# Kernel tuning notes

Measured on AMD Instinct MI355X. Metric: run time of the kernel, lower is better.

## Reference

```python
import jax, jax.numpy as jnp
import numpy as np

T_STEPS = 100
T_EMB = 16
EPS = 1e-8


def sin_emb(t, dim):
    # sinusoidal_time_embedding: [cos(t*f), sin(t*f)] with f = exp(-log(1e4)*i/half)
    half = dim // 2
    freqs = jnp.exp(-jnp.log(jnp.float32(10000.0)) * jnp.arange(half, dtype=jnp.float32) / half)
    a = t.astype(jnp.float32)[:, None] * freqs[None, :]
    return jnp.concatenate([jnp.cos(a), jnp.sin(a)], axis=-1)


def lstm_layer(x_tbf, W_ih, W_hh, b):
    # x_tbf: [T, B, F]; torch gate order i, f, g, o
    B = x_tbf.shape[1]
    H = W_hh.shape[1]

    def step(carry, x_t):
        h, c = carry
        g = x_t @ W_ih.T + h @ W_hh.T + b
        i, f, gg, o = jnp.split(g, 4, axis=-1)
        c = jax.nn.sigmoid(f) * c + jax.nn.sigmoid(i) * jnp.tanh(gg)
        h = jax.nn.sigmoid(o) * jnp.tanh(c)
        return (h, c), h

    z = jnp.zeros((B, H), x_tbf.dtype)
    (h, c), ys = jax.lax.scan(step, (z, z), x_tbf)
    return ys, h


def _forward(x_hist, x_future, y0, turb_idx, pred_steps, init_noise, turb_emb,
             W_ih0, W_hh0, b_ih0, b_hh0, W_ih1, W_hh1, b_ih1, b_hh1,
             W1, b1, W2, b2, W3, b3):
    betas = jnp.linspace(1e-4, 0.02, T_STEPS).astype(jnp.float32)
    alphas = 1.0 - betas
    alpha_bars = jnp.cumprod(alphas)

    B = x_hist.shape[0]
    emb = turb_emb[turb_idx]  # [B, E]
    eh = jnp.broadcast_to(emb[:, None, :], (B, x_hist.shape[1], emb.shape[1]))
    ef = jnp.broadcast_to(emb[:, None, :], (B, x_future.shape[1], emb.shape[1]))
    xh = jnp.concatenate([x_hist, eh], axis=-1).transpose(1, 0, 2)    # [T_in, B, F+E]
    xf = jnp.concatenate([x_future, ef], axis=-1).transpose(1, 0, 2)  # [P, B, exo+E]

    ys0, _ = lstm_layer(xh, W_ih0, W_hh0, b_ih0 + b_hh0)
    _, enc_out = lstm_layer(ys0, W_ih1, W_hh1, b_ih1 + b_hh1)         # [B, H] = h[-1]

    def mlp(x):
        h = jax.nn.relu(x @ W1.T + b1)
        h = jax.nn.relu(h @ W2.T + b2)
        return h @ W3.T + b3

    def ar_step(prev_y, xs):
        exo_t, step, y_init = xs
        cond = jnp.concatenate([enc_out, exo_t, prev_y], axis=1)  # [B, cond_dim]
        h_e = sin_emb(jnp.full((B,), step), T_EMB)

        def dstep(y, t):
            t_e = sin_emb(jnp.full((B,), t), T_EMB)
            eps_hat = mlp(jnp.concatenate([cond, y, t_e, h_e], axis=1))  # [B,1]
            b_t, a_t, ab_t = betas[t], alphas[t], alpha_bars[t]
            pred_x0 = (y - jnp.sqrt(1.0 - ab_t) * eps_hat) / (jnp.sqrt(ab_t) + EPS)
            mean = (y - b_t / (jnp.sqrt(1.0 - ab_t) + EPS) * eps_hat) / (jnp.sqrt(a_t) + EPS)
            # eval mode -> deterministic sampling: posterior noise term is zero
            return jnp.where(t == 0, pred_x0, mean), None

        y, _ = jax.lax.scan(dstep, y_init, jnp.arange(T_STEPS - 1, -1, -1))
        return y, y[:, 0]

    _, seq = jax.lax.scan(ar_step, y0, (xf, jnp.arange(pred_steps), init_noise))
    return seq.T[:, :, None]  # [B, pred_steps, 1]


def setup_inputs() -> dict:
    key = jax.random.key(0)
    ks = list(jax.random.split(key, 24))
    kit = iter(ks)
    B, T_IN, F_IN, EXO, EMB, PRED, HID, NTURB = 1024, 96, 8, 6, 16, 8, 128, 100
    in0 = F_IN + EMB                 # 24
    cond_dim = HID + EXO + EMB + 1   # 151
    in_mlp = cond_dim + 1 + T_EMB + T_EMB  # 184

    def nrm(shape, s=0.05):
        return jax.random.normal(next(kit), shape, jnp.float32) * s

    return {
        'x_hist': jax.random.normal(next(kit), (B, T_IN, F_IN), jnp.float32),
        'x_future': jax.random.normal(next(kit), (B, PRED, EXO), jnp.float32),
        'y0': jnp.zeros((B, 1), jnp.float32),
        'turb_idx': jax.random.randint(next(kit), (B,), 0, NTURB),
        'pred_steps': PRED,
        'init_noise': jax.random.normal(next(kit), (PRED, B, 1), jnp.float32),
        'turb_emb': nrm((NTURB, EMB), 0.1),
        'W_ih0': nrm((4 * HID, in0)), 'W_hh0': nrm((4 * HID, HID)),
        'b_ih0': jnp.zeros((4 * HID,), jnp.float32), 'b_hh0': jnp.zeros((4 * HID,), jnp.float32),
        'W_ih1': nrm((4 * HID, HID)), 'W_hh1': nrm((4 * HID, HID)),
        'b_ih1': jnp.zeros((4 * HID,), jnp.float32), 'b_hh1': jnp.zeros((4 * HID,), jnp.float32),
        'W1': nrm((HID, in_mlp)), 'b1': jnp.zeros((HID,), jnp.float32),
        'W2': nrm((HID, HID)), 'b2': jnp.zeros((HID,), jnp.float32),
        'W3': nrm((1, HID)), 'b3': jnp.zeros((1,), jnp.float32),
    }


def reference(x_hist, x_future, y0, turb_idx, pred_steps, init_noise, turb_emb,
              W_ih0, W_hh0, b_ih0, b_hh0, W_ih1, W_hh1, b_ih1, b_hh1,
              W1, b1, W2, b2, W3, b3):
    return _forward(x_hist, x_future, y0, turb_idx, pred_steps, init_noise, turb_emb,
                    W_ih0, W_hh0, b_ih0, b_hh0, W_ih1, W_hh1, b_ih1, b_hh1,
                    W1, b1, W2, b2, W3, b3)
```

## Files before the change

kernel.cpp:

```cpp
#include <hip/hip_runtime.h>
#include <hip/hip_fp16.h>
#include <stdint.h>


typedef __attribute__((ext_vector_type(2))) _Float16 half2_t;
typedef __attribute__((ext_vector_type(8))) _Float16 v8h;
typedef __attribute__((ext_vector_type(4))) float v4f;

#define DEV __device__ __forceinline__

DEV uint32_t pack2f(float a, float b) {
  __half ha = __float2half_rn(a), hb = __float2half_rn(b);
  return (uint32_t)__half_as_ushort(ha) | ((uint32_t)__half_as_ushort(hb) << 16);
}

DEV float2 up2(uint32_t u) {
  half2_t h = __builtin_bit_cast(half2_t, u);
  return make_float2((float)h.x, (float)h.y);
}

DEV float fast_ex2(float x) {
#if __has_builtin(__builtin_amdgcn_exp2f)
  return __builtin_amdgcn_exp2f(x);
#else
  return exp2f(x);
#endif
}
DEV float fast_rcp(float x) {
#if __has_builtin(__builtin_amdgcn_rcpf)
  return __builtin_amdgcn_rcpf(x);
#else
  return 1.f / x;
#endif
}
DEV float sigm(float x) { return fast_rcp(1.f + fast_ex2(-1.4426950408889634f * x)); }
DEV float tanh_f(float x) {
  return 2.f * fast_rcp(1.f + fast_ex2(-2.8853900817779268f * x)) - 1.f;
}

DEV uint32_t pk_add(uint32_t a, uint32_t b) {
  return __builtin_bit_cast(uint32_t,
      __builtin_bit_cast(half2_t, a) + __builtin_bit_cast(half2_t, b));
}

DEV uint32_t pk_relufma(uint32_t w, uint32_t y, uint32_t b) {
  half2_t r = __builtin_bit_cast(half2_t, w) * __builtin_bit_cast(half2_t, y) +
              __builtin_bit_cast(half2_t, b);
  half2_t z = {(_Float16)0.f, (_Float16)0.f};
#if __has_builtin(__builtin_elementwise_max)
  r = __builtin_elementwise_max(r, z);
#else
  uint32_t u = __builtin_bit_cast(uint32_t, r);
  uint32_t mask = ((u >> 15) & 1u) * 0xFFFFu | ((u >> 31) & 1u) * 0xFFFF0000u;
  r = __builtin_bit_cast(half2_t, u & ~mask);
#endif
  return __builtin_bit_cast(uint32_t, r);
}

DEV uint32_t pk_max0(uint32_t a) {
  half2_t z = {(_Float16)0.f, (_Float16)0.f};
#if __has_builtin(__builtin_elementwise_max)
  return __builtin_bit_cast(uint32_t,
      __builtin_elementwise_max(__builtin_bit_cast(half2_t, a), z));
#else
  uint32_t mask = ((a >> 15) & 1u) * 0xFFFFu | ((a >> 31) & 1u) * 0xFFFF0000u;
  return a & ~mask;
#endif
}

DEV uint32_t cvtpk(float y) {
#if __has_builtin(__builtin_amdgcn_cvt_pkrtz)
  return __builtin_bit_cast(uint32_t, __builtin_amdgcn_cvt_pkrtz(y, y));
#else
  return pack2f(y, y);
#endif
}

DEV uint32_t cvtpk2(float a, float b) {
#if __has_builtin(__builtin_amdgcn_cvt_pkrtz)
  return __builtin_bit_cast(uint32_t, __builtin_amdgcn_cvt_pkrtz(a, b));
#else
  return pack2f(a, b);
#endif
}

DEV half2_t pk_fma2(uint32_t a, uint32_t b, half2_t c) {
  return __builtin_bit_cast(half2_t, a) * __builtin_bit_cast(half2_t, b) + c;
}

static constexpr size_t OFF_XH  = 0;
static constexpr size_t OFF_W0  = 4718592;
static constexpr size_t OFF_BS0 = 4882432;
static constexpr size_t OFF_W1L = 4884480;
static constexpr size_t OFF_BS1 = 5146624;
static constexpr size_t OFF_W2P = 5148672;
static constexpr size_t OFF_ENC = 5181440;
static constexpr size_t OFF_YS0 = 5705728;

__global__ void k_prep_xh(const float* __restrict__ xh, const int* __restrict__ tix,
                          const float* __restrict__ temb, uint32_t* __restrict__ out) {
  int idx = blockIdx.x * 256 + threadIdx.x;
  if (idx >= 96 * 1024 * 12) return;
  int m = idx % 12;
  int tb = idx / 12;
  int b = tb & 1023, t = tb >> 10;
  int k0 = 2 * m, k1 = k0 + 1;
  float v0 = (k0 < 8) ? xh[(b * 96 + t) * 8 + k0] : temb[tix[b] * 16 + (k0 - 8)];
  float v1 = (k1 < 8) ? xh[(b * 96 + t) * 8 + k1] : temb[tix[b] * 16 + (k1 - 8)];
  out[idx] = pack2f(v0, v1);
}

__global__ void k_prep_w(const float* __restrict__ Wih0, const float* __restrict__ Whh0,
                         const float* __restrict__ bih0, const float* __restrict__ bhh0,
                         const float* __restrict__ Wih1, const float* __restrict__ Whh1,
                         const float* __restrict__ bih1, const float* __restrict__ bhh1,
                         const float* __restrict__ W2,
                         uint32_t* __restrict__ w0p, uint32_t* __restrict__ w1p,
                         uint32_t* __restrict__ w2p, float* __restrict__ bs0,
                         float* __restrict__ bs1) {
  int idx = blockIdx.x * 256 + threadIdx.x;
  if (idx < 40960) {
    int w = idx / 5120;
    int r = idx % 5120;
    int T = r / 1280; r %= 1280;
    int f = r / 256;  r %= 256;
    int l = r >> 2, c = r & 3;
    int m = l & 15, qf = l >> 4;
    int g = (m & 3) * 128 + w * 16 + (m >> 2) * 4 + T;
    int k0 = f * 32 + qf * 8 + 2 * c, k1 = k0 + 1;
    float a = (k0 < 24) ? Wih0[g * 24 + k0] : ((k0 < 152) ? Whh0[g * 128 + k0 - 24] : 0.f);
    float b = (k1 < 24) ? Wih0[g * 24 + k1] : ((k1 < 152) ? Whh0[g * 128 + k1 - 24] : 0.f);
    w0p[idx] = pack2f(a, b);
  } else if (idx < 106496) {
    int i = idx - 40960;
    int w = i / 8192;
    int r = i % 8192;
    int T = r / 2048; r %= 2048;
    int f = r / 256;  r %= 256;
    int l = r >> 2, c = r & 3;
    int m = l & 15, qf = l >> 4;
    int g = (m & 3) * 128 + w * 16 + (m >> 2) * 4 + T;
    int k0 = f * 32 + qf * 8 + 2 * c, k1 = k0 + 1;
    float a = (k0 < 128) ? Wih1[g * 128 + k0] : Whh1[g * 128 + k0 - 128];
    float b = (k1 < 128) ? Wih1[g * 128 + k1] : Whh1[g * 128 + k1 - 128];
    w1p[i] = pack2f(a, b);
  } else if (idx < 114688) {
    int i = idx - 106496;
    w2p[i] = pack2f(W2[2 * i], W2[2 * i + 1]);
  } else if (idx < 115200) {
    int i = idx - 114688;
    bs0[i] = bih0[i] + bhh0[i];
  } else if (idx < 115712) {
    int i = idx - 115200;
    bs1[i] = bih1[i] + bhh1[i];
  }
}

__global__ __launch_bounds__(512, 2) void k_lstm0(const uint32_t* __restrict__ xh16,
                                                  const uint32_t* __restrict__ w0A,
                                                  const float* __restrict__ bs0,
                                                  __half* __restrict__ ys0) {
  __shared__ __align__(16) __half inb[2][16][160];
  const int tid = threadIdx.x;
  const int w = tid >> 6, l = tid & 63;
  const int n = l & 15, ql = l >> 4;
  const int ju = w * 16 + ql * 4;
  const int bbase = blockIdx.x * 16;

  uint4 Af[4][5];
#pragma unroll
  for (int T = 0; T < 4; T++)
#pragma unroll
    for (int f = 0; f < 5; f++)
      Af[T][f] = ((const uint4*)w0A)[((w * 4 + T) * 5 + f) * 64 + l];
  float bias[4][4];
#pragma unroll
  for (int T = 0; T < 4; T++)
#pragma unroll
    for (int r = 0; r < 4; r++) bias[T][r] = bs0[r * 128 + ju + T];

  for (int i = tid; i < 2560; i += 512) ((uint32_t*)inb)[i] = 0u;
  __syncthreads();
  if (tid < 192) {
    int b = tid / 12, m = tid % 12;
    ((uint32_t*)&inb[0][b][0])[m] = xh16[(0 * 1024 + bbase + b) * 12 + m];
  }
  float cst[4] = {0.f, 0.f, 0.f, 0.f};
  __syncthreads();

  for (int t = 0; t < 96; t++) {
    const int cur = t & 1, nxt = cur ^ 1;
    uint32_t sx = 0;
    int sb = 0, sm = 0;
    if (t < 95 && tid < 192) {
      sb = tid / 12; sm = tid % 12;
      sx = xh16[((t + 1) * 1024 + bbase + sb) * 12 + sm];
    }
    v4f acc[4];
#pragma unroll
    for (int T = 0; T < 4; T++) acc[T] = (v4f){0.f, 0.f, 0.f, 0.f};
#pragma unroll
    for (int f = 0; f < 5; f++) {
      uint4 bu = *(const uint4*)&inb[cur][n][f * 32 + ql * 8];
      v8h Bv = __builtin_bit_cast(v8h, bu);
#pragma unroll
      for (int T = 0; T < 4; T++)
        acc[T] = __builtin_amdgcn_mfma_f32_16x16x32_f16(
            __builtin_bit_cast(v8h, Af[T][f]), Bv, acc[T], 0, 0, 0);
    }
    float hv[4];
#pragma unroll
    for (int T = 0; T < 4; T++) {
      float gi = acc[T][0] + bias[T][0];
      float gf = acc[T][1] + bias[T][1];
      float gg = acc[T][2] + bias[T][2];
      float go = acc[T][3] + bias[T][3];
      float c = sigm(gf) * cst[T] + sigm(gi) * tanh_f(gg);
      cst[T] = c;
      hv[T] = sigm(go) * tanh_f(c);
    }
    uint32_t h01 = pack2f(hv[0], hv[1]), h23 = pack2f(hv[2], hv[3]);
    *(uint2*)&inb[nxt][n][24 + ju] = make_uint2(h01, h23);
    *(uint2*)((__half*)ys0 + (size_t)(t * 1024 + bbase + n) * 128 + ju) = make_uint2(h01, h23);
    if (t < 95 && tid < 192) ((uint32_t*)&inb[nxt][sb][0])[sm] = sx;
    __syncthreads();
  }
}

__global__ __launch_bounds__(512, 2) void k_lstm1(const uint32_t* __restrict__ ys0u,
                                                  const uint32_t* __restrict__ w1A,
                                                  const float* __restrict__ bs1,
                                                  float* __restrict__ enc) {
  __shared__ __align__(16) __half inb[2][16][264];
  const int tid = threadIdx.x;
  const int w = tid >> 6, l = tid & 63;
  const int n = l & 15, ql = l >> 4;
  const int ju = w * 16 + ql * 4;
  const int bbase = blockIdx.x * 16;
  const int sb = tid >> 5, sc = tid & 31;

  uint4 Af[4][8];
#pragma unroll
  for (int T = 0; T < 4; T++)
#pragma unroll
    for (int f = 0; f < 8; f++)
      Af[T][f] = ((const uint4*)w1A)[((w * 4 + T) * 8 + f) * 64 + l];
  float bias[4][4];
#pragma unroll
  for (int T = 0; T < 4; T++)
#pragma unroll
    for (int r = 0; r < 4; r++) bias[T][r] = bs1[r * 128 + ju + T];

  for (int i = tid; i < 4224; i += 512) ((uint32_t*)inb)[i] = 0u;
  __syncthreads();
  {
    uint2 v = ((const uint2*)ys0u)[(size_t)(0 * 1024 + bbase + sb) * 32 + sc];
    *(uint2*)&inb[0][sb][sc * 4] = v;
  }
  float cst[4] = {0.f, 0.f, 0.f, 0.f};
  __syncthreads();

  for (int t = 0; t < 96; t++) {
    const int cur = t & 1, nxt = cur ^ 1;
    uint2 sv = make_uint2(0u, 0u);
    if (t < 95)
      sv = ((const uint2*)ys0u)[(size_t)((t + 1) * 1024 + bbase + sb) * 32 + sc];
    v4f acc[4];
#pragma unroll
    for (int T = 0; T < 4; T++) acc[T] = (v4f){0.f, 0.f, 0.f, 0.f};
#pragma unroll
    for (int f = 0; f < 8; f++) {
      uint4 bu = *(const uint4*)&inb[cur][n][f * 32 + ql * 8];
      v8h Bv = __builtin_bit_cast(v8h, bu);
#pragma unroll
      for (int T = 0; T < 4; T++)
        acc[T] = __builtin_amdgcn_mfma_f32_16x16x32_f16(
            __builtin_bit_cast(v8h, Af[T][f]), Bv, acc[T], 0, 0, 0);
    }
    float hv[4];
#pragma unroll
    for (int T = 0; T < 4; T++) {
      float gi = acc[T][0] + bias[T][0];
      float gf = acc[T][1] + bias[T][1];
      float gg = acc[T][2] + bias[T][2];
      float go = acc[T][3] + bias[T][3];
      float c = sigm(gf) * cst[T] + sigm(gi) * tanh_f(gg);
      cst[T] = c;
      hv[T] = sigm(go) * tanh_f(c);
    }
    *(uint2*)&inb[nxt][n][128 + ju] = make_uint2(pack2f(hv[0], hv[1]), pack2f(hv[2], hv[3]));
    if (t < 95) *(uint2*)&inb[nxt][sb][sc * 4] = sv;
    if (t == 95)
      *(float4*)&enc[(size_t)(bbase + n) * 128 + ju] = make_float4(hv[0], hv[1], hv[2], hv[3]);
    __syncthreads();
  }
}

__global__ __launch_bounds__(256, 1) void k_diff(
    const float* __restrict__ xfut, const float* __restrict__ y0,
    const int* __restrict__ tix, const float* __restrict__ noise,
    const float* __restrict__ temb, const float* __restrict__ W1,
    const float* __restrict__ b1, const float* __restrict__ b2,
    const float* __restrict__ W3, const float* __restrict__ b3,
    const uint32_t* __restrict__ w2p, const float* __restrict__ enc,
    float* __restrict__ out) {
  __shared__ uint32_t W1sL[128 * 65];
  __shared__ uint32_t W1xL[128 * 29];
  __shared__ uint32_t encPL[16 * 65];
  __shared__ uint32_t embPL[16 * 9];
  __shared__ float teL[100][16];
  __shared__ float2 ccL[100];
  __shared__ __align__(16) __half tprojL[100 * 128];
  __shared__ __half hprojL[8 * 128];
  __shared__ uint32_t encdL[256 * 17];
  __shared__ __align__(16) float partL[2][16][20];

  const int tid = threadIdx.x;
  const int w = tid >> 6, l = tid & 63;
  const int m = l & 15, q = l >> 4;
  const int gbase = blockIdx.x * 16;

  for (int i = tid; i < 128 * 64; i += 256) {
    int r = i >> 6, c = i & 63;
    W1sL[r * 65 + c] = pack2f(W1[r * 184 + 2 * c], W1[r * 184 + 2 * c + 1]);
  }
  for (int i = tid; i < 128 * 28; i += 256) {
    int r = i / 28, c = i % 28;
    W1xL[r * 29 + c] = pack2f(W1[r * 184 + 128 + 2 * c], W1[r * 184 + 129 + 2 * c]);
  }
  for (int i = tid; i < 16 * 64; i += 256) {
    int bq = i >> 6, c = i & 63;
    encPL[bq * 65 + c] = pack2f(enc[(gbase + bq) * 128 + 2 * c],
                                enc[(gbase + bq) * 128 + 2 * c + 1]);
  }
  for (int i = tid; i < 16 * 8; i += 256) {
    int bq = i >> 3, c = i & 7;
    const float* er = temb + tix[gbase + bq] * 16;
    embPL[bq * 9 + c] = pack2f(er[2 * c], er[2 * c + 1]);
  }
  for (int p = tid; p < 1600; p += 256) {
    int tt = p >> 4, i = p & 15;
    float f = expf(-logf(10000.f) * (float)(i & 7) / 8.f);
    float a = (float)tt * f;
    teL[tt][i] = (i < 8) ? cosf(a) : sinf(a);
  }
  for (int qq = tid; qq < 100; qq += 256) {
    float ab = 1.f, beta = 0.f;
    for (int i = 0; i <= qq; i++) {
      beta = 1e-4f + (0.02f - 1e-4f) * (float)i / 99.f;
      ab *= (1.f - beta);
    }
    float cs, cd;
    if (qq == 0) { cs = sqrtf(1.f - ab); cd = 1.f / (sqrtf(ab) + 1e-8f); }
    else { cs = beta / (sqrtf(1.f - ab) + 1e-8f); cd = 1.f / (sqrtf(1.f - beta) + 1e-8f); }
    ccL[qq] = make_float2(cs, cd);
  }
  __syncthreads();

  {
    int k = tid & 127, hs = tid >> 7;
    float wte[16], whe[16];
#pragma unroll
    for (int i = 0; i < 8; i++) {
      float2 a = up2(W1xL[k * 29 + 12 + i]);
      wte[2 * i] = a.x; wte[2 * i + 1] = a.y;
      float2 bqq = up2(W1xL[k * 29 + 20 + i]);
      whe[2 * i] = bqq.x; whe[2 * i + 1] = bqq.y;
    }
    for (int tt = hs * 50; tt < hs * 50 + 50; tt++) {
      float s = 0.f;
#pragma unroll
      for (int i = 0; i < 16; i++) s += wte[i] * teL[tt][i];
      tprojL[tt * 128 + k] = __float2half_rn(s);
    }
    if (hs == 0) {
      for (int ss = 0; ss < 8; ss++) {
        float s = 0.f;
#pragma unroll
        for (int i = 0; i < 16; i++) s += whe[i] * teL[ss][i];
        hprojL[ss * 128 + k] = __float2half_rn(s);
      }
    }
  }

  for (int pi = 0; pi < 16; pi++) {
    int k0 = (pi >> 2) * 32 + q * 8 + (pi & 3) * 2;
    half2_t a0 = {(_Float16)0.f, (_Float16)0.f};
    half2_t a1 = a0;
    const uint32_t* wr0 = &W1sL[k0 * 65];
    const uint32_t* wr1 = &W1sL[(k0 + 1) * 65];
    const uint32_t* ep = &encPL[m * 65];
#pragma unroll 8
    for (int c = 0; c < 64; c++) {
      half2_t e = __builtin_bit_cast(half2_t, ep[c]);
      a0 += __builtin_bit_cast(half2_t, wr0[c]) * e;
      a1 += __builtin_bit_cast(half2_t, wr1[c]) * e;
    }
#pragma unroll
    for (int c = 0; c < 8; c++) {
      half2_t e = __builtin_bit_cast(half2_t, embPL[m * 9 + c]);
      a0 += __builtin_bit_cast(half2_t, W1xL[k0 * 29 + 3 + c]) * e;
      a1 += __builtin_bit_cast(half2_t, W1xL[(k0 + 1) * 29 + 3 + c]) * e;
    }
    float e0 = b1[k0] + (float)a0.x + (float)a0.y;
    float e1 = b1[k0 + 1] + (float)a1.x + (float)a1.y;
    encdL[tid * 17 + pi] = pack2f(e0, e1);
  }

  uint4 Bf[2][4];
  {
    const uint4* w2u4 = (const uint4*)w2p;
#pragma unroll
    for (int j = 0; j < 2; j++)
#pragma unroll
      for (int f = 0; f < 4; f++)
        Bf[j][f] = w2u4[((2 * w + j) * 16 + m) * 16 + f * 4 + q];
  }
  uint32_t b2P[4], w3P[4];
#pragma unroll
  for (int j = 0; j < 2; j++) {
    int tt = 2 * w + j;
    b2P[2 * j]     = pack2f(b2[tt * 16 + q * 4 + 0], b2[tt * 16 + q * 4 + 1]);
    b2P[2 * j + 1] = pack2f(b2[tt * 16 + q * 4 + 2], b2[tt * 16 + q * 4 + 3]);
    w3P[2 * j]     = pack2f(W3[tt * 16 + q * 4 + 0], W3[tt * 16 + q * 4 + 1]);
    w3P[2 * j + 1] = pack2f(W3[tt * 16 + q * 4 + 2], W3[tt * 16 + q * 4 + 3]);
  }
  const float b3v = b3[0];
  const int pslot = w * 4 + q;

  uint32_t w1yP[16];
#pragma unroll
  for (int pi = 0; pi < 16; pi++) {
    int k0 = (pi >> 2) * 32 + q * 8 + (pi & 3) * 2;
    uint32_t ua = W1xL[k0 * 29 + 11];
    uint32_t ub = W1xL[(k0 + 1) * 29 + 11];
    w1yP[pi] = (ua >> 16) | (ub & 0xFFFF0000u);
  }

  float prev_y = y0[gbase + m];
  __syncthreads();

  float y = 0.f;
  float2 ccv = make_float2(0.f, 0.f);
  uint32_t bph[16], bt[16];
  const v4f zf = (v4f){0.f, 0.f, 0.f, 0.f};

#define DSTEP(t_, PB)                                                          \
  do {                                                                         \
    const int tn_ = ((t_) > 0) ? (t_) - 1 : 0;                                 \
    const uint4* tb_ = (const uint4*)(tprojL + tn_ * 128 + q * 8);             \
    uint4 t0 = tb_[0], t1 = tb_[4], t2 = tb_[8], t3 = tb_[12];                 \
    float2 ccn_ = ccL[tn_];                                                    \
    const uint32_t yP = cvtpk(y);                                              \
    uint4 au[4];                                                               \
    _Pragma("unroll")                                                          \
    for (int f = 0; f < 4; f++) {                                              \
      au[f].x = pk_relufma(w1yP[4 * f + 0], yP, bt[4 * f + 0]);                \
      au[f].y = pk_relufma(w1yP[4 * f + 1], yP, bt[4 * f + 1]);                \
      au[f].z = pk_relufma(w1yP[4 * f + 2], yP, bt[4 * f + 2]);                \
      au[f].w = pk_relufma(w1yP[4 * f + 3], yP, bt[4 * f + 3]);                \
    }                                                                          \
                             \
    v4f a0 = __builtin_amdgcn_mfma_f32_16x16x32_f16(                           \
        __builtin_bit_cast(v8h, Bf[0][0]), __builtin_bit_cast(v8h, au[0]), zf, 0, 0, 0); \
    v4f b0 = __builtin_amdgcn_mfma_f32_16x16x32_f16(                           \
        __builtin_bit_cast(v8h, Bf[0][1]), __builtin_bit_cast(v8h, au[1]), zf, 0, 0, 0); \
    v4f a1 = __builtin_amdgcn_mfma_f32_16x16x32_f16(                           \
        __builtin_bit_cast(v8h, Bf[1][0]), __builtin_bit_cast(v8h, au[0]), zf, 0, 0, 0); \
    v4f b1x = __builtin_amdgcn_mfma_f32_16x16x32_f16(                          \
        __builtin_bit_cast(v8h, Bf[1][1]), __builtin_bit_cast(v8h, au[1]), zf, 0, 0, 0); \
    a0 = __builtin_amdgcn_mfma_f32_16x16x32_f16(                               \
        __builtin_bit_cast(v8h, Bf[0][2]), __builtin_bit_cast(v8h, au[2]), a0, 0, 0, 0); \
    b0 = __builtin_amdgcn_mfma_f32_16x16x32_f16(                               \
        __builtin_bit_cast(v8h, Bf[0][3]), __builtin_bit_cast(v8h, au[3]), b0, 0, 0, 0); \
    a1 = __builtin_amdgcn_mfma_f32_16x16x32_f16(                               \
        __builtin_bit_cast(v8h, Bf[1][2]), __builtin_bit_cast(v8h, au[2]), a1, 0, 0, 0); \
    b1x = __builtin_amdgcn_mfma_f32_16x16x32_f16(                              \
        __builtin_bit_cast(v8h, Bf[1][3]), __builtin_bit_cast(v8h, au[3]), b1x, 0, 0, 0); \
    v4f c0 = a0 + b0, c1 = a1 + b1x;                                           \
              \
    half2_t run = {(_Float16)0.f, (_Float16)0.f};                              \
    {                                                                          \
      uint32_t h01 = pk_max0(pk_add(cvtpk2(c0[0], c0[1]), b2P[0]));            \
      uint32_t h23 = pk_max0(pk_add(cvtpk2(c0[2], c0[3]), b2P[1]));            \
      run = pk_fma2(h01, w3P[0], run);                                         \
      run = pk_fma2(h23, w3P[1], run);                                         \
      uint32_t g01 = pk_max0(pk_add(cvtpk2(c1[0], c1[1]), b2P[2]));            \
      uint32_t g23 = pk_max0(pk_add(cvtpk2(c1[2], c1[3]), b2P[3]));            \
      run = pk_fma2(g01, w3P[2], run);                                         \
      run = pk_fma2(g23, w3P[3], run);                                         \
    }                                                                          \
    partL[PB][m][pslot] = (float)run.x + (float)run.y;                         \
                                         \
    bt[0] = pk_add(bph[0], t0.x);   bt[1] = pk_add(bph[1], t0.y);              \
    bt[2] = pk_add(bph[2], t0.z);   bt[3] = pk_add(bph[3], t0.w);              \
    bt[4] = pk_add(bph[4], t1.x);   bt[5] = pk_add(bph[5], t1.y);              \
    bt[6] = pk_add(bph[6], t1.z);   bt[7] = pk_add(bph[7], t1.w);              \
    bt[8] = pk_add(bph[8], t2.x);   bt[9] = pk_add(bph[9], t2.y);              \
    bt[10] = pk_add(bph[10], t2.z); bt[11] = pk_add(bph[11], t2.w);            \
    bt[12] = pk_add(bph[12], t3.x); bt[13] = pk_add(bph[13], t3.y);            \
    bt[14] = pk_add(bph[14], t3.z); bt[15] = pk_add(bph[15], t3.w);            \
    __syncthreads();                                                           \
    const v4f* pl_ = (const v4f*)&partL[PB][m][0];                             \
    v4f p0_ = pl_[0], p1_ = pl_[1], p2_ = pl_[2], p3_ = pl_[3];                \
    v4f ps_ = (p0_ + p1_) + (p2_ + p3_);                                       \
    float eps_ = b3v + ((ps_[0] + ps_[1]) + (ps_[2] + ps_[3]));                \
    y = (y - ccv.x * eps_) * ccv.y;                                            \
    ccv = ccn_;                                                                \
  } while (0)

  for (int s = 0; s < 8; s++) {
    float yn = noise[s * 1024 + gbase + m];
    float xf[6];
#pragma unroll
    for (int i = 0; i < 6; i++) xf[i] = xfut[((gbase + m) * 8 + s) * 6 + i];
#pragma unroll
    for (int pi = 0; pi < 16; pi++) {
      int k0 = (pi >> 2) * 32 + q * 8 + (pi & 3) * 2;
      float2 ed = up2(encdL[tid * 17 + pi]);
      float e0 = ed.x, e1 = ed.y;
#pragma unroll
      for (int c = 0; c < 3; c++) {
        float2 w0v = up2(W1xL[k0 * 29 + c]);
        float2 w1v = up2(W1xL[(k0 + 1) * 29 + c]);
        e0 += w0v.x * xf[2 * c] + w0v.y * xf[2 * c + 1];
        e1 += w1v.x * xf[2 * c] + w1v.y * xf[2 * c + 1];
      }
      e0 += up2(W1xL[k0 * 29 + 11]).x * prev_y;
      e1 += up2(W1xL[(k0 + 1) * 29 + 11]).x * prev_y;
      e0 += (float)hprojL[s * 128 + k0];
      e1 += (float)hprojL[s * 128 + k0 + 1];
      bph[pi] = pack2f(e0, e1);
    }

    y = yn;
    {
      const uint4* tb = (const uint4*)(tprojL + 99 * 128 + q * 8);
      uint4 t0 = tb[0], t1 = tb[4], t2 = tb[8], t3 = tb[12];
      bt[0] = pk_add(bph[0], t0.x);   bt[1] = pk_add(bph[1], t0.y);
      bt[2] = pk_add(bph[2], t0.z);   bt[3] = pk_add(bph[3], t0.w);
      bt[4] = pk_add(bph[4], t1.x);   bt[5] = pk_add(bph[5], t1.y);
      bt[6] = pk_add(bph[6], t1.z);   bt[7] = pk_add(bph[7], t1.w);
      bt[8] = pk_add(bph[8], t2.x);   bt[9] = pk_add(bph[9], t2.y);
      bt[10] = pk_add(bph[10], t2.z); bt[11] = pk_add(bph[11], t2.w);
      bt[12] = pk_add(bph[12], t3.x); bt[13] = pk_add(bph[13], t3.y);
      bt[14] = pk_add(bph[14], t3.z); bt[15] = pk_add(bph[15], t3.w);
    }
    ccv = ccL[99];

    for (int it = 0; it < 50; it++) {
      DSTEP(99 - 2 * it, 0);
      DSTEP(98 - 2 * it, 1);
    }

    if (w == 0 && l < 16) out[(gbase + l) * 8 + s] = y;
    prev_y = y;
  }
#undef DSTEP
}

extern "C" void kernel_launch(void* const* d_in, const int* in_sizes, int n_in,
                              void* d_out, int out_size, void* d_ws, size_t ws_size,
                              hipStream_t stream) {
  const float* x_hist    = (const float*)d_in[0];
  const float* x_future  = (const float*)d_in[1];
  const float* y0        = (const float*)d_in[2];
  const int*   turb_idx  = (const int*)d_in[3];
  const float* init_noise = (const float*)d_in[5];
  const float* turb_emb  = (const float*)d_in[6];
  const float* W_ih0     = (const float*)d_in[7];
  const float* W_hh0     = (const float*)d_in[8];
  const float* b_ih0     = (const float*)d_in[9];
  const float* b_hh0     = (const float*)d_in[10];
  const float* W_ih1     = (const float*)d_in[11];
  const float* W_hh1     = (const float*)d_in[12];
  const float* b_ih1     = (const float*)d_in[13];
  const float* b_hh1     = (const float*)d_in[14];
  const float* W1        = (const float*)d_in[15];
  const float* b1        = (const float*)d_in[16];
  const float* W2        = (const float*)d_in[17];
  const float* b2        = (const float*)d_in[18];
  const float* W3        = (const float*)d_in[19];
  const float* b3        = (const float*)d_in[20];

  char* ws = (char*)d_ws;
  uint32_t* xh16 = (uint32_t*)(ws + OFF_XH);
  uint32_t* w0p  = (uint32_t*)(ws + OFF_W0);
  float*    bs0  = (float*)(ws + OFF_BS0);
  uint32_t* w1p  = (uint32_t*)(ws + OFF_W1L);
  float*    bs1  = (float*)(ws + OFF_BS1);
  uint32_t* w2p  = (uint32_t*)(ws + OFF_W2P);
  float*    encf = (float*)(ws + OFF_ENC);
  __half*   ys0h = (__half*)(ws + OFF_YS0);

  k_prep_xh<<<4608, 256, 0, stream>>>(x_hist, turb_idx, turb_emb, xh16);
  k_prep_w<<<452, 256, 0, stream>>>(W_ih0, W_hh0, b_ih0, b_hh0,
                                    W_ih1, W_hh1, b_ih1, b_hh1,
                                    W2, w0p, w1p, w2p, bs0, bs1);
  k_lstm0<<<64, 512, 0, stream>>>(xh16, w0p, bs0, ys0h);
  k_lstm1<<<64, 512, 0, stream>>>((const uint32_t*)ys0h, w1p, bs1, encf);
  k_diff<<<64, 256, 0, stream>>>(x_future, y0, turb_idx, init_noise, turb_emb,
                                 W1, b1, b2, W3, b3, w2p, encf, (float*)d_out);
}
```

Baseline: 638.5 us.

## Precompute diffusion time projections in prep kernel and halve diffusion block size

The time-embedding projections, step-embedding projections and schedule coefficients move out of the per-block setup of k_diff into the prep kernel, which writes them to workspace. k_diff now reads them from global memory (cached) inside the denoising loop. The diffusion kernel drops from 4 to 2 waves per block, and each wave now does 4 MFMA tiles of W2 instead of 2. This shrinks the cross-wave reduction and the barrier cost on every serial denoising step. The risks are extra global-load latency on the critical serial path and more register pressure per wave.

```diff
diff --git a/kernel.cpp b/kernel.cpp
--- a/kernel.cpp
+++ b/kernel.cpp
@@ -96,6 +96,9 @@
 static constexpr size_t OFF_W2P = 5148672;
 static constexpr size_t OFF_ENC = 5181440;
 static constexpr size_t OFF_YS0 = 5705728;
+static constexpr size_t OFF_TPJ = 30871552;
+static constexpr size_t OFF_HPJ = 30897152;
+static constexpr size_t OFF_CC  = 30899200;
 
 __global__ void k_prep_xh(const float* __restrict__ xh, const int* __restrict__ tix,
                           const float* __restrict__ temb, uint32_t* __restrict__ out) {
@@ -114,10 +117,11 @@
                          const float* __restrict__ bih0, const float* __restrict__ bhh0,
                          const float* __restrict__ Wih1, const float* __restrict__ Whh1,
                          const float* __restrict__ bih1, const float* __restrict__ bhh1,
-                         const float* __restrict__ W2,
+                         const float* __restrict__ W2, const float* __restrict__ W1,
                          uint32_t* __restrict__ w0p, uint32_t* __restrict__ w1p,
                          uint32_t* __restrict__ w2p, float* __restrict__ bs0,
-                         float* __restrict__ bs1) {
+                         float* __restrict__ bs1, uint32_t* __restrict__ tpj,
+                         uint32_t* __restrict__ hpj, float2* __restrict__ ccg) {
   int idx = blockIdx.x * 256 + threadIdx.x;
   if (idx < 40960) {
     int w = idx / 5120;
@@ -153,6 +157,59 @@
   } else if (idx < 115712) {
     int i = idx - 115200;
     bs1[i] = bih1[i] + bhh1[i];
+  } else if (idx < 122112) {
+    int i = idx - 115712;
+    int t = i / 64;
+    int r = i % 64;
+    int q = r / 16, pi = r % 16;
+    int k0 = (pi >> 2) * 32 + q * 8 + (pi & 3) * 2;
+    float te[16];
+#pragma unroll
+    for (int j = 0; j < 8; j++) {
+      float f = expf(-logf(10000.f) * (float)j / 8.f);
+      float a = (float)t * f;
+      te[j] = cosf(a);
+      te[j + 8] = sinf(a);
+    }
+    float s0 = 0.f, s1 = 0.f;
+#pragma unroll
+    for (int j = 0; j < 16; j++) {
+      s0 += W1[k0 * 184 + 152 + j] * te[j];
+      s1 += W1[(k0 + 1) * 184 + 152 + j] * te[j];
+    }
+    tpj[i] = pack2f((float)__half2float(__float2half_rn(s0)),
+                    (float)__half2float(__float2half_rn(s1)));
+  } else if (idx < 122624) {
+    int i = idx - 122112;
+    int s = i / 64;
+    int kp = i % 64;
+    float te[16];
+#pragma unroll
+    for (int j = 0; j < 8; j++) {
+      float f = expf(-logf(10000.f) * (float)j / 8.f);
+      float a = (float)s * f;
+      te[j] = cosf(a);
+      te[j + 8] = sinf(a);
+    }
+    float s0 = 0.f, s1 = 0.f;
+#pragma unroll
+    for (int j = 0; j < 16; j++) {
+      s0 += W1[(2 * kp) * 184 + 168 + j] * te[j];
+      s1 += W1[(2 * kp + 1) * 184 + 168 + j] * te[j];
+    }
+    hpj[i] = pack2f((float)__half2float(__float2half_rn(s0)),
+                    (float)__half2float(__float2half_rn(s1)));
+  } else if (idx < 122724) {
+    int qq = idx - 122624;
+    float ab = 1.f, beta = 0.f;
+    for (int i = 0; i <= qq; i++) {
+      beta = 1e-4f + (0.02f - 1e-4f) * (float)i / 99.f;
+      ab *= (1.f - beta);
+    }
+    float cs, cd;
+    if (qq == 0) { cs = sqrtf(1.f - ab); cd = 1.f / (sqrtf(ab) + 1e-8f); }
+    else { cs = beta / (sqrtf(1.f - ab) + 1e-8f); cd = 1.f / (sqrtf(1.f - beta) + 1e-8f); }
+    ccg[qq] = make_float2(cs, cd);
   }
 }
 
@@ -296,92 +353,47 @@
   }
 }
 
-__global__ __launch_bounds__(256, 1) void k_diff(
+__global__ __launch_bounds__(128, 1) void k_diff(
     const float* __restrict__ xfut, const float* __restrict__ y0,
     const int* __restrict__ tix, const float* __restrict__ noise,
     const float* __restrict__ temb, const float* __restrict__ W1,
     const float* __restrict__ b1, const float* __restrict__ b2,
     const float* __restrict__ W3, const float* __restrict__ b3,
     const uint32_t* __restrict__ w2p, const float* __restrict__ enc,
-    float* __restrict__ out) {
+    const uint32_t* __restrict__ tpj, const uint32_t* __restrict__ hpj,
+    const float2* __restrict__ ccG, float* __restrict__ out) {
   __shared__ uint32_t W1sL[128 * 65];
   __shared__ uint32_t W1xL[128 * 29];
   __shared__ uint32_t encPL[16 * 65];
   __shared__ uint32_t embPL[16 * 9];
-  __shared__ float teL[100][16];
-  __shared__ float2 ccL[100];
-  __shared__ __align__(16) __half tprojL[100 * 128];
-  __shared__ __half hprojL[8 * 128];
-  __shared__ uint32_t encdL[256 * 17];
-  __shared__ __align__(16) float partL[2][16][20];
+  __shared__ uint32_t encdL[128 * 17];
+  __shared__ __align__(16) float partL[2][16][12];
 
   const int tid = threadIdx.x;
   const int w = tid >> 6, l = tid & 63;
   const int m = l & 15, q = l >> 4;
   const int gbase = blockIdx.x * 16;
-
-  for (int i = tid; i < 128 * 64; i += 256) {
+  const uint4* tpj4 = (const uint4*)tpj;
+
+  for (int i = tid; i < 128 * 64; i += 128) {
     int r = i >> 6, c = i & 63;
     W1sL[r * 65 + c] = pack2f(W1[r * 184 + 2 * c], W1[r * 184 + 2 * c + 1]);
   }
-  for (int i = tid; i < 128 * 28; i += 256) {
+  for (int i = tid; i < 128 * 28; i += 128) {
     int r = i / 28, c = i % 28;
     W1xL[r * 29 + c] = pack2f(W1[r * 184 + 128 + 2 * c], W1[r * 184 + 129 + 2 * c]);
   }
-  for (int i = tid; i < 16 * 64; i += 256) {
+  for (int i = tid; i < 16 * 64; i += 128) {
     int bq = i >> 6, c = i & 63;
     encPL[bq * 65 + c] = pack2f(enc[(gbase + bq) * 128 + 2 * c],
                                 enc[(gbase + bq) * 128 + 2 * c + 1]);
   }
-  for (int i = tid; i < 16 * 8; i += 256) {
+  for (int i = tid; i < 16 * 8; i += 128) {
     int bq = i >> 3, c = i & 7;
     const float* er = temb + tix[gbase + bq] * 16;
     embPL[bq * 9 + c] = pack2f(er[2 * c], er[2 * c + 1]);
   }
-  for (int p = tid; p < 1600; p += 256) {
-    int tt = p >> 4, i = p & 15;
-    float f = expf(-logf(10000.f) * (float)(i & 7) / 8.f);
-    float a = (float)tt * f;
-    teL[tt][i] = (i < 8) ? cosf(a) : sinf(a);
-  }
-  for (int qq = tid; qq < 100; qq += 256) {
-    float ab = 1.f, beta = 0.f;
-    for (int i = 0; i <= qq; i++) {
-      beta = 1e-4f + (0.02f - 1e-4f) * (float)i / 99.f;
-      ab *= (1.f - beta);
-    }
-    float cs, cd;
-    if (qq == 0) { cs = sqrtf(1.f - ab); cd = 1.f / (sqrtf(ab) + 1e-8f); }
-    else { cs = beta / (sqrtf(1.f - ab) + 1e-8f); cd = 1.f / (sqrtf(1.f - beta) + 1e-8f); }
-    ccL[qq] = make_float2(cs, cd);
-  }
   __syncthreads();
-
-  {
-    int k = tid & 127, hs = tid >> 7;
-    float wte[16], whe[16];
-#pragma unroll
-    for (int i = 0; i < 8; i++) {
-      float2 a = up2(W1xL[k * 29 + 12 + i]);
-      wte[2 * i] = a.x; wte[2 * i + 1] = a.y;
-      float2 bqq = up2(W1xL[k * 29 + 20 + i]);
-      whe[2 * i] = bqq.x; whe[2 * i + 1] = bqq.y;
-    }
-    for (int tt = hs * 50; tt < hs * 50 + 50; tt++) {
-      float s = 0.f;
-#pragma unroll
-      for (int i = 0; i < 16; i++) s += wte[i] * teL[tt][i];
-      tprojL[tt * 128 + k] = __float2half_rn(s);
-    }
-    if (hs == 0) {
-      for (int ss = 0; ss < 8; ss++) {
-        float s = 0.f;
-#pragma unroll
-        for (int i = 0; i < 16; i++) s += whe[i] * teL[ss][i];
-        hprojL[ss * 128 + k] = __float2half_rn(s);
-      }
-    }
-  }
 
   for (int pi = 0; pi < 16; pi++) {
     int k0 = (pi >> 2) * 32 + q * 8 + (pi & 3) * 2;
@@ -407,19 +419,19 @@
     encdL[tid * 17 + pi] = pack2f(e0, e1);
   }
 
-  uint4 Bf[2][4];
+  uint4 Bf[4][4];
   {
     const uint4* w2u4 = (const uint4*)w2p;
 #pragma unroll
-    for (int j = 0; j < 2; j++)
+    for (int j = 0; j < 4; j++)
 #pragma unroll
       for (int f = 0; f < 4; f++)
-        Bf[j][f] = w2u4[((2 * w + j) * 16 + m) * 16 + f * 4 + q];
-  }
-  uint32_t b2P[4], w3P[4];
-#pragma unroll
-  for (int j = 0; j < 2; j++) {
-    int tt = 2 * w + j;
+        Bf[j][f] = w2u4[((4 * w + j) * 16 + m) * 16 + f * 4 + q];
+  }
+  uint32_t b2P[8], w3P[8];
+#pragma unroll
+  for (int j = 0; j < 4; j++) {
+    int tt = 4 * w + j;
     b2P[2 * j]     = pack2f(b2[tt * 16 + q * 4 + 0], b2[tt * 16 + q * 4 + 1]);
     b2P[2 * j + 1] = pack2f(b2[tt * 16 + q * 4 + 2], b2[tt * 16 + q * 4 + 3]);
     w3P[2 * j]     = pack2f(W3[tt * 16 + q * 4 + 0], W3[tt * 16 + q * 4 + 1]);
@@ -448,9 +460,9 @@
 #define DSTEP(t_, PB)                                                          \
   do {                                                                         \
     const int tn_ = ((t_) > 0) ? (t_) - 1 : 0;                                 \
-    const uint4* tb_ = (const uint4*)(tprojL + tn_ * 128 + q * 8);             \
-    uint4 t0 = tb_[0], t1 = tb_[4], t2 = tb_[8], t3 = tb_[12];                 \
-    float2 ccn_ = ccL[tn_];                                                    \
+    const uint4* tg_ = tpj4 + (size_t)(tn_ * 4 + q) * 4;    \
+    uint4 t0 = tg_[0], t1 = tg_[1], t2 = tg_[2], t3 = tg_[3];                  \
+    float2 ccn_ = ccG[tn_];                                                    \
     const uint32_t yP = cvtpk(y);                                              \
     uint4 au[4];                                                               \
     _Pragma("unroll")                                                          \
@@ -460,37 +472,49 @@
       au[f].z = pk_relufma(w1yP[4 * f + 2], yP, bt[4 * f + 2]);                \
       au[f].w = pk_relufma(w1yP[4 * f + 3], yP, bt[4 * f + 3]);                \
     }                                                                          \
-                             \
-    v4f a0 = __builtin_amdgcn_mfma_f32_16x16x32_f16(                           \
-        __builtin_bit_cast(v8h, Bf[0][0]), __builtin_bit_cast(v8h, au[0]), zf, 0, 0, 0); \
-    v4f b0 = __builtin_amdgcn_mfma_f32_16x16x32_f16(                           \
-        __builtin_bit_cast(v8h, Bf[0][1]), __builtin_bit_cast(v8h, au[1]), zf, 0, 0, 0); \
-    v4f a1 = __builtin_amdgcn_mfma_f32_16x16x32_f16(                           \
-        __builtin_bit_cast(v8h, Bf[1][0]), __builtin_bit_cast(v8h, au[0]), zf, 0, 0, 0); \
-    v4f b1x = __builtin_amdgcn_mfma_f32_16x16x32_f16(                          \
-        __builtin_bit_cast(v8h, Bf[1][1]), __builtin_bit_cast(v8h, au[1]), zf, 0, 0, 0); \
-    a0 = __builtin_amdgcn_mfma_f32_16x16x32_f16(                               \
-        __builtin_bit_cast(v8h, Bf[0][2]), __builtin_bit_cast(v8h, au[2]), a0, 0, 0, 0); \
-    b0 = __builtin_amdgcn_mfma_f32_16x16x32_f16(                               \
-        __builtin_bit_cast(v8h, Bf[0][3]), __builtin_bit_cast(v8h, au[3]), b0, 0, 0, 0); \
-    a1 = __builtin_amdgcn_mfma_f32_16x16x32_f16(                               \
-        __builtin_bit_cast(v8h, Bf[1][2]), __builtin_bit_cast(v8h, au[2]), a1, 0, 0, 0); \
-    b1x = __builtin_amdgcn_mfma_f32_16x16x32_f16(                              \
-        __builtin_bit_cast(v8h, Bf[1][3]), __builtin_bit_cast(v8h, au[3]), b1x, 0, 0, 0); \
-    v4f c0 = a0 + b0, c1 = a1 + b1x;                                           \
+                            \
+    v4f aA[4], aB[4];                                                          \
+    _Pragma("unroll")                                                          \
+    for (int j = 0; j < 4; j++)                                                \
+      aA[j] = __builtin_amdgcn_mfma_f32_16x16x32_f16(                          \
+          __builtin_bit_cast(v8h, Bf[j][0]), __builtin_bit_cast(v8h, au[0]),   \
+          zf, 0, 0, 0);                                                        \
+    _Pragma("unroll")                                                          \
+    for (int j = 0; j < 4; j++)                                                \
+      aB[j] = __builtin_amdgcn_mfma_f32_16x16x32_f16(                          \
+          __builtin_bit_cast(v8h, Bf[j][1]), __builtin_bit_cast(v8h, au[1]),   \
+          zf, 0, 0, 0);                                                        \
+    _Pragma("unroll")                                                          \
+    for (int j = 0; j < 4; j++)                                                \
+      aA[j] = __builtin_amdgcn_mfma_f32_16x16x32_f16(                          \
+          __builtin_bit_cast(v8h, Bf[j][2]), __builtin_bit_cast(v8h, au[2]),   \
+          aA[j], 0, 0, 0);                                                     \
+    _Pragma("unroll")                                                          \
+    for (int j = 0; j < 4; j++)                                                \
+      aB[j] = __builtin_amdgcn_mfma_f32_16x16x32_f16(                          \
+          __builtin_bit_cast(v8h, Bf[j][3]), __builtin_bit_cast(v8h, au[3]),   \
+          aB[j], 0, 0, 0);                                                     \
               \
-    half2_t run = {(_Float16)0.f, (_Float16)0.f};                              \
-    {                                                                          \
-      uint32_t h01 = pk_max0(pk_add(cvtpk2(c0[0], c0[1]), b2P[0]));            \
-      uint32_t h23 = pk_max0(pk_add(cvtpk2(c0[2], c0[3]), b2P[1]));            \
-      run = pk_fma2(h01, w3P[0], run);                                         \
-      run = pk_fma2(h23, w3P[1], run);                                         \
-      uint32_t g01 = pk_max0(pk_add(cvtpk2(c1[0], c1[1]), b2P[2]));            \
-      uint32_t g23 = pk_max0(pk_add(cvtpk2(c1[2], c1[3]), b2P[3]));            \
-      run = pk_fma2(g01, w3P[2], run);                                         \
-      run = pk_fma2(g23, w3P[3], run);                                         \
+    half2_t runA = {(_Float16)0.f, (_Float16)0.f};                             \
+    half2_t runB = runA;                                                       \
+    _Pragma("unroll")                                                          \
+    for (int j = 0; j < 2; j++) {                                              \
+      v4f c = aA[j] + aB[j];                                                   \
+      uint32_t h01 = pk_max0(pk_add(cvtpk2(c[0], c[1]), b2P[2 * j]));          \
+      uint32_t h23 = pk_max0(pk_add(cvtpk2(c[2], c[3]), b2P[2 * j + 1]));      \
+      runA = pk_fma2(h01, w3P[2 * j], runA);                                   \
+      runA = pk_fma2(h23, w3P[2 * j + 1], runA);                               \
     }                                                                          \
-    partL[PB][m][pslot] = (float)run.x + (float)run.y;                         \
+    _Pragma("unroll")                                                          \
+    for (int j = 2; j < 4; j++) {                                              \
+      v4f c = aA[j] + aB[j];                                                   \
+      uint32_t h01 = pk_max0(pk_add(cvtpk2(c[0], c[1]), b2P[2 * j]));          \
+      uint32_t h23 = pk_max0(pk_add(cvtpk2(c[2], c[3]), b2P[2 * j + 1]));      \
+      runB = pk_fma2(h01, w3P[2 * j], runB);                                   \
+      runB = pk_fma2(h23, w3P[2 * j + 1], runB);                               \
+    }                                                                          \
+    partL[PB][m][pslot] = ((float)runA.x + (float)runA.y) +                    \
+                          ((float)runB.x + (float)runB.y);                     \
                                          \
     bt[0] = pk_add(bph[0], t0.x);   bt[1] = pk_add(bph[1], t0.y);              \
     bt[2] = pk_add(bph[2], t0.z);   bt[3] = pk_add(bph[3], t0.w);              \
@@ -502,8 +526,7 @@
     bt[14] = pk_add(bph[14], t3.z); bt[15] = pk_add(bph[15], t3.w);            \
     __syncthreads();                                                           \
     const v4f* pl_ = (const v4f*)&partL[PB][m][0];                             \
-    v4f p0_ = pl_[0], p1_ = pl_[1], p2_ = pl_[2], p3_ = pl_[3];                \
-    v4f ps_ = (p0_ + p1_) + (p2_ + p3_);                                       \
+    v4f ps_ = pl_[0] + pl_[1];                                                 \
     float eps_ = b3v + ((ps_[0] + ps_[1]) + (ps_[2] + ps_[3]));                \
     y = (y - ccv.x * eps_) * ccv.y;                                            \
     ccv = ccn_;                                                                \
@@ -528,15 +551,16 @@
       }
       e0 += up2(W1xL[k0 * 29 + 11]).x * prev_y;
       e1 += up2(W1xL[(k0 + 1) * 29 + 11]).x * prev_y;
-      e0 += (float)hprojL[s * 128 + k0];
-      e1 += (float)hprojL[s * 128 + k0 + 1];
+      float2 hh = up2(hpj[s * 64 + (k0 >> 1)]);
+      e0 += hh.x;
+      e1 += hh.y;
       bph[pi] = pack2f(e0, e1);
     }
 
     y = yn;
     {
-      const uint4* tb = (const uint4*)(tprojL + 99 * 128 + q * 8);
-      uint4 t0 = tb[0], t1 = tb[4], t2 = tb[8], t3 = tb[12];
+      const uint4* tg = tpj4 + (size_t)(99 * 4 + q) * 4;
+      uint4 t0 = tg[0], t1 = tg[1], t2 = tg[2], t3 = tg[3];
       bt[0] = pk_add(bph[0], t0.x);   bt[1] = pk_add(bph[1], t0.y);
       bt[2] = pk_add(bph[2], t0.z);   bt[3] = pk_add(bph[3], t0.w);
       bt[4] = pk_add(bph[4], t1.x);   bt[5] = pk_add(bph[5], t1.y);
@@ -546,7 +570,7 @@
       bt[12] = pk_add(bph[12], t3.x); bt[13] = pk_add(bph[13], t3.y);
       bt[14] = pk_add(bph[14], t3.z); bt[15] = pk_add(bph[15], t3.w);
     }
-    ccv = ccL[99];
+    ccv = ccG[99];
 
     for (int it = 0; it < 50; it++) {
       DSTEP(99 - 2 * it, 0);
@@ -592,13 +616,18 @@
   uint32_t* w2p  = (uint32_t*)(ws + OFF_W2P);
   float*    encf = (float*)(ws + OFF_ENC);
   __half*   ys0h = (__half*)(ws + OFF_YS0);
+  uint32_t* tpjw = (uint32_t*)(ws + OFF_TPJ);
+  uint32_t* hpjw = (uint32_t*)(ws + OFF_HPJ);
+  float2*   ccw  = (float2*)(ws + OFF_CC);
 
   k_prep_xh<<<4608, 256, 0, stream>>>(x_hist, turb_idx, turb_emb, xh16);
-  k_prep_w<<<452, 256, 0, stream>>>(W_ih0, W_hh0, b_ih0, b_hh0,
+  k_prep_w<<<480, 256, 0, stream>>>(W_ih0, W_hh0, b_ih0, b_hh0,
                                     W_ih1, W_hh1, b_ih1, b_hh1,
-                                    W2, w0p, w1p, w2p, bs0, bs1);
+                                    W2, W1, w0p, w1p, w2p, bs0, bs1,
+                                    tpjw, hpjw, ccw);
   k_lstm0<<<64, 512, 0, stream>>>(xh16, w0p, bs0, ys0h);
   k_lstm1<<<64, 512, 0, stream>>>((const uint32_t*)ys0h, w1p, bs1, encf);
-  k_diff<<<64, 256, 0, stream>>>(x_future, y0, turb_idx, init_noise, turb_emb,
-                                 W1, b1, b2, W3, b3, w2p, encf, (float*)d_out);
-}
+  k_diff<<<64, 128, 0, stream>>>(x_future, y0, turb_idx, init_noise, turb_emb,
+                                 W1, b1, b2, W3, b3, w2p, encf,
+                                 tpjw, hpjw, ccw, (float*)d_out);
+}
```

New measurement: 702.0 us. 9.9% more time.
